# Performance work log

Measured on AMD Instinct MI355X. Metric: run time of the kernel, lower is better.

## Reference

```python
import jax, jax.numpy as jnp
import numpy as np

T = 2048           # tokens (single prefill sequence)
HIDDEN = 2048
H = 16             # num heads
D_NOPE = 128
D_ROPE = 64
D_V = 128
KV_LORA = 512
EPS = 1e-6
ROPE_THETA = 10000.0


def setup_inputs() -> dict:
    key = jax.random.key(0)
    ks = jax.random.split(key, 7)
    s = 0.02
    return {
        "positions": jnp.arange(T, dtype=jnp.int64) if jax.config.jax_enable_x64 else jnp.arange(T, dtype=jnp.int32),
        "hidden_states": jax.random.normal(ks[0], (T, HIDDEN), dtype=jnp.float32),
        "w_q": jax.random.normal(ks[1], (HIDDEN, H * (D_NOPE + D_ROPE)), dtype=jnp.float32) * s,
        "w_kv_a": jax.random.normal(ks[2], (HIDDEN, KV_LORA + D_ROPE), dtype=jnp.float32) * s,
        "kv_a_ln_w": jax.random.uniform(ks[3], (KV_LORA,), dtype=jnp.float32, minval=0.5, maxval=1.5),
        "w_kv_b": jax.random.normal(ks[4], (KV_LORA, H * (D_NOPE + D_V)), dtype=jnp.float32) * s,
        "w_o": jax.random.normal(ks[5], (H * D_V, HIDDEN), dtype=jnp.float32) * s,
    }


def _rms_norm(x, w):
    var = jnp.mean(jnp.square(x), axis=-1, keepdims=True)
    return x * jax.lax.rsqrt(var + EPS) * w


def _rope_nonneox(x, positions):
    # x: [..., D_ROPE], GPT-J (interleaved) style rotation
    inv_freq = 1.0 / (ROPE_THETA ** (jnp.arange(0, D_ROPE, 2, dtype=jnp.float32) / D_ROPE))
    freqs = positions.astype(jnp.float32)[:, None] * inv_freq  # [T, D_ROPE//2]
    cos, sin = jnp.cos(freqs), jnp.sin(freqs)
    # broadcast over head dim if present
    while cos.ndim < x.ndim:
        cos, sin = cos[:, None], sin[:, None]
    x1, x2 = x[..., 0::2], x[..., 1::2]
    o1 = x1 * cos - x2 * sin
    o2 = x2 * cos + x1 * sin
    return jnp.stack([o1, o2], axis=-1).reshape(x.shape)


def reference(positions, hidden_states, w_q, w_kv_a, kv_a_ln_w, w_kv_b, w_o):
    scaling = (D_NOPE + D_ROPE) ** -0.5
    # q projection (q_lora_rank is None branch)
    q = (hidden_states @ w_q).reshape(T, H, D_NOPE + D_ROPE)
    q_nope, q_pe = q[..., :D_NOPE], q[..., D_NOPE:]
    # compressed KV latent
    latent = hidden_states @ w_kv_a                 # [T, KV_LORA + D_ROPE]
    kv_a = _rms_norm(latent[:, :KV_LORA], kv_a_ln_w)
    k_pe = latent[:, KV_LORA:]                      # [T, D_ROPE], shared across heads
    # decompress to per-head k_nope and v (kv_b_proj)
    kv = (kv_a @ w_kv_b).reshape(T, H, D_NOPE + D_V)
    k_nope, v = kv[..., :D_NOPE], kv[..., D_NOPE:]
    # non-neox RoPE
    q_pe = _rope_nonneox(q_pe, positions)
    k_pe = _rope_nonneox(k_pe, positions)           # [T, D_ROPE]
    # concat rope parts (k_pe broadcast over heads)
    q_full = jnp.concatenate([q_nope, q_pe], axis=-1)                         # [T,H,192]
    k_full = jnp.concatenate([k_nope, jnp.broadcast_to(k_pe[:, None, :], (T, H, D_ROPE))], axis=-1)
    # causal MHA
    scores = jnp.einsum("qhd,khd->hqk", q_full, k_full) * scaling
    causal = positions[:, None] >= positions[None, :]
    scores = jnp.where(causal[None], scores, -jnp.inf)
    attn = jax.nn.softmax(scores, axis=-1)
    out = jnp.einsum("hqk,khd->qhd", attn, v).reshape(T, H * D_V)
    return out @ w_o
```

## Files before the change

### kernel.cpp

```cpp
#include <hip/hip_runtime.h>
#include <hip/hip_bf16.h>
#include <stdint.h>

#define T_SEQ   2048
#define NHEAD   16
#define NPAD1   3712

typedef short bf16x8  __attribute__((ext_vector_type(8)));
typedef float f32x4   __attribute__((ext_vector_type(4)));
typedef float f32x16  __attribute__((ext_vector_type(16)));

__device__ __forceinline__ unsigned short f2bf(float f) {
  union { float f; uint32_t u; } v; v.f = f;
  uint32_t u = v.u;
  uint32_t r = u + 0x7FFF + ((u >> 16) & 1);
  return (unsigned short)(r >> 16);
}

__device__ __forceinline__ void async16(const void* g, void* l) {
  __builtin_amdgcn_global_load_lds(
      (const __attribute__((address_space(1))) void*)g,
      (__attribute__((address_space(3))) void*)l, 16, 0, 0);
}

__device__ __forceinline__ void tr32(const float* __restrict__ in,
    unsigned short* __restrict__ out, int R, int C, int bx, int by,
    float (*tile)[33], int tid) {
  int r0 = bx * 32, c0 = by * 32;
  int tx = tid & 31, ty = tid >> 5;
  for (int i = 0; i < 4; i++)
    tile[ty + i * 8][tx] = in[(size_t)(r0 + ty + i * 8) * C + c0 + tx];
  __syncthreads();
  for (int i = 0; i < 4; i++) {
    int c = ty + i * 8;
    out[(size_t)(c0 + c) * R + r0 + tx] = f2bf(tile[tx][c]);
  }
}

__global__ __launch_bounds__(256) void prep_kernel(
    const float* __restrict__ hs, const float* __restrict__ w_q,
    const float* __restrict__ w_kv_a, const float* __restrict__ w_kv_b,
    const float* __restrict__ w_o, const int* __restrict__ positions,
    unsigned short* __restrict__ hs_bf, unsigned short* __restrict__ wcat_t,
    unsigned short* __restrict__ wkvb_t, unsigned short* __restrict__ wo_t,
    float* __restrict__ rope_tab) {
  __shared__ float tile[32][33];
  int bid = blockIdx.x, tid = threadIdx.x;
  if (bid < 4096) {
    int i = (bid * 256 + tid) * 4;
    float4 v = *(const float4*)(hs + i);
    ushort4 o; o.x = f2bf(v.x); o.y = f2bf(v.y); o.z = f2bf(v.z); o.w = f2bf(v.w);
    *(ushort4*)(hs_bf + i) = o;
  } else if (bid < 4096 + 6144) {
    int l = bid - 4096;
    tr32(w_q, wcat_t, 2048, 3072, l & 63, l >> 6, tile, tid);
  } else if (bid < 4096 + 6144 + 1152) {
    int l = bid - (4096 + 6144);
    tr32(w_kv_a, wcat_t + (size_t)3072 * 2048, 2048, 576, l & 63, l >> 6, tile, tid);
  } else if (bid < 4096 + 6144 + 1152 + 2048) {
    int l = bid - (4096 + 6144 + 1152);
    tr32(w_kv_b, wkvb_t, 512, 4096, l & 15, l >> 4, tile, tid);
  } else if (bid < 4096 + 6144 + 1152 + 2048 + 4096) {
    int l = bid - (4096 + 6144 + 1152 + 2048);
    tr32(w_o, wo_t, 2048, 2048, l & 63, l >> 6, tile, tid);
  } else if (bid < 17600) {
    int l = bid - (4096 + 6144 + 1152 + 2048 + 4096);
    uint4 z = (uint4){0, 0, 0, 0};
    *(uint4*)(wcat_t + (size_t)3648 * 2048 + (size_t)(l * 256 + tid) * 8) = z;
  } else {
    int l = bid - 17600;
    int t = l * 8 + (tid >> 5), p = tid & 31;
    float pos = (float)positions[t];
    float inv_freq = powf(10000.f, -(float)(2 * p) / 64.f);
    float c, s; sincosf(pos * inv_freq, &s, &c);
    rope_tab[(size_t)t * 64 + 2 * p]     = c;
    rope_tab[(size_t)t * 64 + 2 * p + 1] = s;
  }
}

template<int TM, int EPI>
__global__ __launch_bounds__(256) void gemm_bt_kernel(
    const unsigned short* __restrict__ A, const unsigned short* __restrict__ B,
    void* __restrict__ Cv, int M, int N, int K,
    unsigned short* __restrict__ q_full, const float* __restrict__ rope_tab) {
  constexpr int MT = TM / 32;
  __shared__ __align__(16) unsigned short Asm[2][TM * 64];
  __shared__ __align__(16) unsigned short Bsm[2][128 * 64];
  int tid = threadIdx.x, wid = tid >> 6, lane = tid & 63;
  int lrow = lane & 15, lquad = lane >> 4;
  int m0 = blockIdx.x * TM, n0 = blockIdx.y * 128;
  int wm = (wid & 1) * (TM / 2), wn = (wid >> 1) * 64;

  int row_s = tid >> 3;
  int cc_s = (tid & 7) ^ (row_s & 7);
  const unsigned short* Ag[MT];
  const unsigned short* Bg[4];
  #pragma unroll
  for (int p = 0; p < MT; p++) Ag[p] = A + (size_t)(m0 + row_s + p * 32) * K + cc_s * 8;
  #pragma unroll
  for (int p = 0; p < 4; p++)  Bg[p] = B + (size_t)(n0 + row_s + p * 32) * K + cc_s * 8;

  f32x4 acc[MT][4];
  #pragma unroll
  for (int i = 0; i < MT; i++)
    #pragma unroll
    for (int j = 0; j < 4; j++) acc[i][j] = (f32x4){0.f,0.f,0.f,0.f};

  #pragma unroll
  for (int p = 0; p < MT; p++) async16(Ag[p], &Asm[0][(tid + p * 256) * 8]);
  #pragma unroll
  for (int p = 0; p < 4; p++)  async16(Bg[p], &Bsm[0][(tid + p * 256) * 8]);

  int cur = 0;
  for (int k0 = 0; k0 < K; k0 += 64) {
    __syncthreads();
    if (k0 + 64 < K) {
      int nxt = cur ^ 1, kk = k0 + 64;
      #pragma unroll
      for (int p = 0; p < MT; p++) async16(Ag[p] + kk, &Asm[nxt][(tid + p * 256) * 8]);
      #pragma unroll
      for (int p = 0; p < 4; p++)  async16(Bg[p] + kk, &Bsm[nxt][(tid + p * 256) * 8]);
    }
    const unsigned short* As = Asm[cur];
    const unsigned short* Bs = Bsm[cur];
    int xr = (lrow & 7);
    #pragma unroll
    for (int kk = 0; kk < 2; kk++) {
      int cz = ((kk * 4 + lquad) ^ xr) * 8;
      bf16x8 af[MT], bfr[4];
      #pragma unroll
      for (int mt = 0; mt < MT; mt++)
        af[mt] = *(const bf16x8*)(As + (wm + mt * 16 + lrow) * 64 + cz);
      #pragma unroll
      for (int nt = 0; nt < 4; nt++)
        bfr[nt] = *(const bf16x8*)(Bs + (wn + nt * 16 + lrow) * 64 + cz);
      #pragma unroll
      for (int mt = 0; mt < MT; mt++)
        #pragma unroll
        for (int nt = 0; nt < 4; nt++)
          acc[mt][nt] = __builtin_amdgcn_mfma_f32_16x16x32_bf16(af[mt], bfr[nt], acc[mt][nt], 0, 0, 0);
    }
    cur ^= 1;
  }

  if constexpr (EPI == 2) {
    const float scaling = 0.07216878364870323f;
    float* qlat = (float*)Cv;
    #pragma unroll
    for (int nt = 0; nt < 4; nt++) {
      int colb = n0 + wn + nt * 16;
      if (colb >= 3072) {
        int col = colb - 3072 + lrow;
        #pragma unroll
        for (int mt = 0; mt < MT; mt++) {
          int row = m0 + wm + mt * 16 + lquad * 4;
          #pragma unroll
          for (int r = 0; r < 4; r++)
            qlat[(size_t)(row + r) * 640 + col] = acc[mt][nt][r];
        }
      } else {
        int h = colb / 192;
        int hm = colb - h * 192;
        unsigned short* qh = q_full + (size_t)h * T_SEQ * 192;
        if (hm < 128) {
          #pragma unroll
          for (int mt = 0; mt < MT; mt++) {
            int row = m0 + wm + mt * 16 + lquad * 4;
            #pragma unroll
            for (int r = 0; r < 4; r++)
              qh[(size_t)(row + r) * 192 + hm + lrow] = f2bf(acc[mt][nt][r] * scaling);
          }
        } else {
          int p2 = (hm - 128 + lrow) & ~1;
          int odd = lrow & 1;
          #pragma unroll
          for (int mt = 0; mt < MT; mt++) {
            int row = m0 + wm + mt * 16 + lquad * 4;
            #pragma unroll
            for (int r = 0; r < 4; r++) {
              int rg = row + r;
              float c = rope_tab[(size_t)rg * 64 + p2];
              float s = rope_tab[(size_t)rg * 64 + p2 + 1];
              float own = acc[mt][nt][r];
              float oth = __shfl_xor(own, 1, 64);
              float o = odd ? (own * c + oth * s)
                            : (own * c - oth * s);
              qh[(size_t)rg * 192 + hm + lrow] = f2bf(o * scaling);
            }
          }
        }
      }
    }
  } else {
    #pragma unroll
    for (int mt = 0; mt < MT; mt++)
      #pragma unroll
      for (int nt = 0; nt < 4; nt++) {
        int row = m0 + wm + mt * 16 + lquad * 4;
        int col = n0 + wn + nt * 16 + lrow;
        #pragma unroll
        for (int r = 0; r < 4; r++) {
          if (EPI == 1)
            ((unsigned short*)Cv)[(size_t)(row + r) * N + col] = f2bf(acc[mt][nt][r]);
          else
            ((float*)Cv)[(size_t)(row + r) * N + col] = acc[mt][nt][r];
        }
      }
  }
}

__global__ __launch_bounds__(256) void postproc1_kernel(
    const float* __restrict__ q_lat,
    const float* __restrict__ ln_w,
    const float* __restrict__ rope_tab,
    unsigned short* __restrict__ kv_a,
    unsigned short* __restrict__ k_pe)
{
  int t = blockIdx.x, tid = threadIdx.x;
  const float* row = q_lat + (size_t)t * 640;

  float v0 = row[tid], v1 = row[256 + tid];
  float ss = v0 * v0 + v1 * v1;
  for (int m = 1; m < 64; m <<= 1) ss += __shfl_xor(ss, m, 64);
  __shared__ float red[4];
  if ((tid & 63) == 0) red[tid >> 6] = ss;
  __shared__ float kro[64];
  if (tid < 32) {
    float c = rope_tab[(size_t)t * 64 + 2 * tid];
    float s = rope_tab[(size_t)t * 64 + 2 * tid + 1];
    float x1 = row[512 + 2 * tid], x2 = row[512 + 2 * tid + 1];
    kro[2 * tid]     = x1 * c - x2 * s;
    kro[2 * tid + 1] = x2 * c + x1 * s;
  }
  __syncthreads();
  float rstd = rsqrtf((red[0] + red[1] + red[2] + red[3]) * (1.f / 512.f) + 1e-6f);
  kv_a[(size_t)t * 512 + tid]       = f2bf(v0 * rstd * ln_w[tid]);
  kv_a[(size_t)t * 512 + 256 + tid] = f2bf(v1 * rstd * ln_w[256 + tid]);
  if (tid < 64) k_pe[(size_t)t * 64 + tid] = f2bf(kro[tid]);
}

__global__ __launch_bounds__(256) void kvpost_kernel(
    const unsigned short* __restrict__ kv_b,
    unsigned short* __restrict__ v_t) {
  __shared__ unsigned short tile[32][41];
  int l = blockIdx.x, tid = threadIdx.x;
  int h = l >> 8, t0 = (l & 63) * 32, d0 = ((l >> 6) & 3) * 32;
  int tx = tid & 31, ty = tid >> 5;
  for (int i = 0; i < 4; i++)
    tile[ty + i * 8][tx] = kv_b[(size_t)(t0 + ty + i * 8) * 4096 + h * 256 + 128 + d0 + tx];
  __syncthreads();
  for (int i = 0; i < 4; i++)
    v_t[((size_t)h * 128 + d0 + ty + i * 8) * T_SEQ + t0 + tx] = tile[tx][ty + i * 8];
}

#define PP 76
__global__ __launch_bounds__(256, 2) void flash_kernel(
    const unsigned short* __restrict__ q_full,
    const unsigned short* __restrict__ kv_b,
    const unsigned short* __restrict__ k_pe,
    const unsigned short* __restrict__ v_t,
    unsigned short* __restrict__ attn_out)
{
  __shared__ __align__(16) unsigned short Ksm[2][1536 * 8];
  __shared__ __align__(16) unsigned short Vsm[1024 * 8];
  __shared__ __align__(16) unsigned short Psm[64 * PP];
  __shared__ float Lred[2][64];
  int h = blockIdx.x;
  int y = blockIdx.y;
  int qb = (y < 16) ? (31 - y) : (y - 16);
  int tid = threadIdx.x, wid = tid >> 6, lane = tid & 63;
  int l31 = lane & 31, l5 = lane >> 5, x7 = l31 & 7;
  int rq = wid & 1, kq = wid >> 1;

  const unsigned short* vh = v_t + (size_t)h * 128 * T_SEQ;

  const unsigned short* pK[6]; int sK[6];
  #pragma unroll
  for (int j = 0; j < 6; j++) {
    int s = tid + j * 256, row = s / 24, cm = s - row * 24;
    int c = cm ^ (row & 7);
    if (c < 16) { pK[j] = kv_b + (size_t)row * 4096 + h * 256 + c * 8; sK[j] = 64 * 4096; }
    else        { pK[j] = k_pe + (size_t)row * 64 + (c - 16) * 8;      sK[j] = 64 * 64; }
  }
  int gV[4];
  #pragma unroll
  for (int j = 0; j < 4; j++) {
    int s = tid + j * 256, d = s >> 3;
    gV[j] = d * T_SEQ + ((s & 7) ^ (d & 7)) * 8;
  }
  int kxo[12];
  #pragma unroll
  for (int kc = 0; kc < 12; kc++)
    kxo[kc] = (kq * 32 + l31) * 192 + ((kc * 2 + l5) ^ x7) * 8;
  int vxb[2];
  #pragma unroll
  for (int ntv = 0; ntv < 2; ntv++) vxb[ntv] = (kq * 64 + ntv * 32 + l31) * 64;

  bf16x8 qf[12];
  {
    const unsigned short* qrow =
        q_full + ((size_t)h * T_SEQ + qb * 64 + rq * 32 + l31) * 192 + l5 * 8;
    #pragma unroll
    for (int kc = 0; kc < 12; kc++) qf[kc] = *(const bf16x8*)(qrow + kc * 16);
  }
  f32x16 oacc[2];
  for (int i = 0; i < 2; i++) oacc[i] = (f32x16)(0.f);
  float lsum[16];
  #pragma unroll
  for (int r = 0; r < 16; r++) lsum[r] = 0.f;
  int rl[16];
  #pragma unroll
  for (int r = 0; r < 16; r++) rl[r] = (r & 3) + 8 * (r >> 2) + 4 * l5;

  #pragma unroll
  for (int j = 0; j < 6; j++) async16(pK[j], &Ksm[0][(tid + j * 256) * 8]);

  int cur = 0;
  for (int kb = 0; kb <= qb; kb++) {
    __syncthreads();
    {
      const unsigned short* vb = vh + kb * 64;
      #pragma unroll
      for (int j = 0; j < 4; j++) async16(vb + gV[j], &Vsm[(tid + j * 256) * 8]);
    }
    const unsigned short* Ks = Ksm[cur];
    f32x16 sacc = (f32x16)(0.f);
    #pragma unroll
    for (int kc = 0; kc < 12; kc++) {
      bf16x8 kf = *(const bf16x8*)(Ks + kxo[kc]);
      sacc = __builtin_amdgcn_mfma_f32_32x32x16_bf16(qf[kc], kf, sacc, 0, 0, 0);
    }
    if (kb == qb) {
      int col_g = kb * 64 + kq * 32 + l31;
      int row_b = qb * 64 + rq * 32;
      #pragma unroll
      for (int r = 0; r < 16; r++)
        if (col_g > row_b + rl[r]) sacc[r] = -1e30f;
    }
    #pragma unroll
    for (int r = 0; r < 16; r++) {
      float p = __expf(sacc[r]);
      sacc[r] = p;
      lsum[r] += p;
    }
    #pragma unroll
    for (int r = 0; r < 16; r++)
      Psm[(rq * 32 + rl[r]) * PP + kq * 32 + l31] = f2bf(sacc[r]);
    __syncthreads();
    if (kb < qb) {
      #pragma unroll
      for (int j = 0; j < 6; j++)
        async16(pK[j] + (size_t)(kb + 1) * sK[j], &Ksm[cur ^ 1][(tid + j * 256) * 8]);
    }
    #pragma unroll
    for (int kc = 0; kc < 4; kc++) {
      bf16x8 pf = *(const bf16x8*)(Psm + (rq * 32 + l31) * PP + kc * 16 + l5 * 8);
      #pragma unroll
      for (int ntv = 0; ntv < 2; ntv++) {
        bf16x8 vf = *(const bf16x8*)(Vsm + vxb[ntv] + ((kc * 2 + l5) ^ x7) * 8);
        oacc[ntv] = __builtin_amdgcn_mfma_f32_32x32x16_bf16(pf, vf, oacc[ntv], 0, 0, 0);
      }
    }
    cur ^= 1;
  }

  #pragma unroll
  for (int r = 0; r < 16; r++) {
    float s = lsum[r];
    s += __shfl_xor(s, 1, 64);
    s += __shfl_xor(s, 2, 64);
    s += __shfl_xor(s, 4, 64);
    s += __shfl_xor(s, 8, 64);
    s += __shfl_xor(s, 16, 64);
    lsum[r] = s;
  }
  if (l31 == 0)
    #pragma unroll
    for (int r = 0; r < 16; r++) Lred[kq][rq * 32 + rl[r]] = lsum[r];
  __syncthreads();
  #pragma unroll
  for (int r = 0; r < 16; r++) {
    int row_l = rq * 32 + rl[r];
    float inv = 1.f / (Lred[0][row_l] + Lred[1][row_l]);
    int row_g = qb * 64 + row_l;
    #pragma unroll
    for (int ntv = 0; ntv < 2; ntv++)
      attn_out[(size_t)row_g * 2048 + h * 128 + kq * 64 + ntv * 32 + l31] =
          f2bf(oacc[ntv][r] * inv);
  }
}

extern "C" void kernel_launch(void* const* d_in, const int* in_sizes, int n_in,
                              void* d_out, int out_size, void* d_ws, size_t ws_size,
                              hipStream_t stream) {
  const int*   positions = (const int*)d_in[0];
  const float* hs     = (const float*)d_in[1];
  const float* w_q    = (const float*)d_in[2];
  const float* w_kv_a = (const float*)d_in[3];
  const float* ln_w   = (const float*)d_in[4];
  const float* w_kv_b = (const float*)d_in[5];
  const float* w_o    = (const float*)d_in[6];
  float* out = (float*)d_out;

  char* ws = (char*)d_ws;
  size_t off = 0;
  auto alloc = [&](size_t bytes) { void* p = ws + off; off += (bytes + 255) & ~(size_t)255; return p; };
  unsigned short* hs_bf   = (unsigned short*)alloc((size_t)2048 * 2048 * 2);
  unsigned short* wcat_t  = (unsigned short*)alloc((size_t)NPAD1 * 2048 * 2);
  float*          q_lat   = (float*)alloc((size_t)2048 * 640 * 4);
  unsigned short* kv_a_bf = (unsigned short*)alloc((size_t)2048 * 512 * 2);
  unsigned short* wkvb_t  = (unsigned short*)alloc((size_t)4096 * 512 * 2);
  unsigned short* kv_b    = (unsigned short*)alloc((size_t)2048 * 4096 * 2);
  unsigned short* q_full  = (unsigned short*)alloc((size_t)NHEAD * 2048 * 192 * 2);
  unsigned short* k_pe    = (unsigned short*)alloc((size_t)2048 * 64 * 2);
  unsigned short* v_t     = (unsigned short*)alloc((size_t)NHEAD * 128 * 2048 * 2);
  unsigned short* attn_o  = (unsigned short*)alloc((size_t)2048 * 2048 * 2);
  unsigned short* wo_t    = (unsigned short*)alloc((size_t)2048 * 2048 * 2);
  float*          rope_tab= (float*)alloc((size_t)2048 * 64 * 4);

  prep_kernel<<<17856, 256, 0, stream>>>(hs, w_q, w_kv_a, w_kv_b, w_o, positions,
                                         hs_bf, wcat_t, wkvb_t, wo_t, rope_tab);
  gemm_bt_kernel<128, 2><<<dim3(16, 29), 256, 0, stream>>>(
      hs_bf, wcat_t, q_lat, 2048, NPAD1, 2048, q_full, rope_tab);
  postproc1_kernel<<<2048, 256, 0, stream>>>(q_lat, ln_w, rope_tab, kv_a_bf, k_pe);
  gemm_bt_kernel<128, 1><<<dim3(16, 32), 256, 0, stream>>>(
      kv_a_bf, wkvb_t, kv_b, 2048, 4096, 512, nullptr, nullptr);
  kvpost_kernel<<<4096, 256, 0, stream>>>(kv_b, v_t);
  flash_kernel<<<dim3(16, 32), 256, 0, stream>>>(q_full, kv_b, k_pe, v_t, attn_o);
  gemm_bt_kernel<64, 0><<<dim3(32, 16), 256, 0, stream>>>(
      attn_o, wo_t, out, 2048, 2048, 2048, nullptr, nullptr);
}
```

Baseline: 252.7 us.

## Split long causal query blocks across two workgroups with partial-sum combine

```diff
diff --git a/kernel.cpp b/kernel.cpp
--- a/kernel.cpp
+++ b/kernel.cpp
@@ -254,20 +254,30 @@
 }
 
 #define PP 76
+#define PSTRIDE 8256
 __global__ __launch_bounds__(256, 2) void flash_kernel(
     const unsigned short* __restrict__ q_full,
     const unsigned short* __restrict__ kv_b,
     const unsigned short* __restrict__ k_pe,
     const unsigned short* __restrict__ v_t,
-    unsigned short* __restrict__ attn_out)
+    unsigned short* __restrict__ attn_out,
+    float* __restrict__ part)
 {
   __shared__ __align__(16) unsigned short Ksm[2][1536 * 8];
   __shared__ __align__(16) unsigned short Vsm[1024 * 8];
   __shared__ __align__(16) unsigned short Psm[64 * PP];
   __shared__ float Lred[2][64];
   int h = blockIdx.x;
-  int y = blockIdx.y;
-  int qb = (y < 16) ? (31 - y) : (y - 16);
+  int j = blockIdx.y;
+  int qb, k0t, k1t, pidx;
+  if (j < 32) {
+    qb = 16 + (j >> 1);
+    int mid = (qb + 1) >> 1;
+    if (j & 1) { k0t = mid; k1t = qb + 1; } else { k0t = 0; k1t = mid; }
+    pidx = (h * 16 + (qb - 16)) * 2 + (j & 1);
+  } else {
+    qb = 47 - j; k0t = 0; k1t = qb + 1; pidx = -1;
+  }
   int tid = threadIdx.x, wid = tid >> 6, lane = tid & 63;
   int l31 = lane & 31, l5 = lane >> 5, x7 = l31 & 7;
   int rq = wid & 1, kq = wid >> 1;
@@ -276,17 +286,17 @@
 
   const unsigned short* pK[6]; int sK[6];
   #pragma unroll
-  for (int j = 0; j < 6; j++) {
-    int s = tid + j * 256, row = s / 24, cm = s - row * 24;
+  for (int j2 = 0; j2 < 6; j2++) {
+    int s = tid + j2 * 256, row = s / 24, cm = s - row * 24;
     int c = cm ^ (row & 7);
-    if (c < 16) { pK[j] = kv_b + (size_t)row * 4096 + h * 256 + c * 8; sK[j] = 64 * 4096; }
-    else        { pK[j] = k_pe + (size_t)row * 64 + (c - 16) * 8;      sK[j] = 64 * 64; }
+    if (c < 16) { pK[j2] = kv_b + (size_t)row * 4096 + h * 256 + c * 8; sK[j2] = 64 * 4096; }
+    else        { pK[j2] = k_pe + (size_t)row * 64 + (c - 16) * 8;      sK[j2] = 64 * 64; }
   }
   int gV[4];
   #pragma unroll
-  for (int j = 0; j < 4; j++) {
-    int s = tid + j * 256, d = s >> 3;
-    gV[j] = d * T_SEQ + ((s & 7) ^ (d & 7)) * 8;
+  for (int j2 = 0; j2 < 4; j2++) {
+    int s = tid + j2 * 256, d = s >> 3;
+    gV[j2] = d * T_SEQ + ((s & 7) ^ (d & 7)) * 8;
   }
   int kxo[12];
   #pragma unroll
@@ -313,15 +323,16 @@
   for (int r = 0; r < 16; r++) rl[r] = (r & 3) + 8 * (r >> 2) + 4 * l5;
 
   #pragma unroll
-  for (int j = 0; j < 6; j++) async16(pK[j], &Ksm[0][(tid + j * 256) * 8]);
+  for (int j2 = 0; j2 < 6; j2++)
+    async16(pK[j2] + (size_t)k0t * sK[j2], &Ksm[0][(tid + j2 * 256) * 8]);
 
   int cur = 0;
-  for (int kb = 0; kb <= qb; kb++) {
+  for (int kb = k0t; kb < k1t; kb++) {
     __syncthreads();
     {
       const unsigned short* vb = vh + kb * 64;
       #pragma unroll
-      for (int j = 0; j < 4; j++) async16(vb + gV[j], &Vsm[(tid + j * 256) * 8]);
+      for (int j2 = 0; j2 < 4; j2++) async16(vb + gV[j2], &Vsm[(tid + j2 * 256) * 8]);
     }
     const unsigned short* Ks = Ksm[cur];
     f32x16 sacc = (f32x16)(0.f);
@@ -347,10 +358,10 @@
     for (int r = 0; r < 16; r++)
       Psm[(rq * 32 + rl[r]) * PP + kq * 32 + l31] = f2bf(sacc[r]);
     __syncthreads();
-    if (kb < qb) {
-      #pragma unroll
-      for (int j = 0; j < 6; j++)
-        async16(pK[j] + (size_t)(kb + 1) * sK[j], &Ksm[cur ^ 1][(tid + j * 256) * 8]);
+    if (kb + 1 < k1t) {
+      #pragma unroll
+      for (int j2 = 0; j2 < 6; j2++)
+        async16(pK[j2] + (size_t)(kb + 1) * sK[j2], &Ksm[cur ^ 1][(tid + j2 * 256) * 8]);
     }
     #pragma unroll
     for (int kc = 0; kc < 4; kc++) {
@@ -378,15 +389,49 @@
     #pragma unroll
     for (int r = 0; r < 16; r++) Lred[kq][rq * 32 + rl[r]] = lsum[r];
   __syncthreads();
-  #pragma unroll
-  for (int r = 0; r < 16; r++) {
-    int row_l = rq * 32 + rl[r];
-    float inv = 1.f / (Lred[0][row_l] + Lred[1][row_l]);
-    int row_g = qb * 64 + row_l;
-    #pragma unroll
-    for (int ntv = 0; ntv < 2; ntv++)
-      attn_out[(size_t)row_g * 2048 + h * 128 + kq * 64 + ntv * 32 + l31] =
-          f2bf(oacc[ntv][r] * inv);
+  if (pidx < 0) {
+    #pragma unroll
+    for (int r = 0; r < 16; r++) {
+      int row_l = rq * 32 + rl[r];
+      float inv = 1.f / (Lred[0][row_l] + Lred[1][row_l]);
+      int row_g = qb * 64 + row_l;
+      #pragma unroll
+      for (int ntv = 0; ntv < 2; ntv++)
+        attn_out[(size_t)row_g * 2048 + h * 128 + kq * 64 + ntv * 32 + l31] =
+            f2bf(oacc[ntv][r] * inv);
+    }
+  } else {
+    float* pb = part + (size_t)pidx * PSTRIDE;
+    #pragma unroll
+    for (int r = 0; r < 16; r++) {
+      int row_l = rq * 32 + rl[r];
+      #pragma unroll
+      for (int ntv = 0; ntv < 2; ntv++)
+        pb[row_l * 128 + kq * 64 + ntv * 32 + l31] = oacc[ntv][r];
+    }
+    if (tid < 64) pb[8192 + tid] = Lred[0][tid] + Lred[1][tid];
+  }
+}
+
+__global__ __launch_bounds__(256) void combine_kernel(
+    const float* __restrict__ part, unsigned short* __restrict__ attn_out) {
+  int bx = blockIdx.x;
+  int h = bx >> 4, q16 = bx & 15, qb = 16 + q16;
+  size_t b0 = (size_t)((h * 16 + q16) * 2) * PSTRIDE;
+  size_t b1 = b0 + PSTRIDE;
+  __shared__ float Ls[64];
+  int tid = threadIdx.x;
+  if (tid < 64) Ls[tid] = part[b0 + 8192 + tid] + part[b1 + 8192 + tid];
+  __syncthreads();
+  for (int i = tid; i < 2048; i += 256) {
+    float4 a = *(const float4*)(part + b0 + (size_t)i * 4);
+    float4 c = *(const float4*)(part + b1 + (size_t)i * 4);
+    int row = i >> 5;
+    float inv = 1.f / Ls[row];
+    ushort4 o;
+    o.x = f2bf((a.x + c.x) * inv); o.y = f2bf((a.y + c.y) * inv);
+    o.z = f2bf((a.z + c.z) * inv); o.w = f2bf((a.w + c.w) * inv);
+    *(ushort4*)(attn_out + (size_t)(qb * 64 + row) * 2048 + h * 128 + (i & 31) * 4) = o;
   }
 }
 
@@ -417,6 +462,7 @@
   unsigned short* attn_o  = (unsigned short*)alloc((size_t)2048 * 2048 * 2);
   unsigned short* wo_t    = (unsigned short*)alloc((size_t)2048 * 2048 * 2);
   float*          rope_tab= (float*)alloc((size_t)2048 * 64 * 4);
+  float*          part    = (float*)alloc((size_t)512 * PSTRIDE * 4);
 
   prep_kernel<<<17856, 256, 0, stream>>>(hs, w_q, w_kv_a, w_kv_b, w_o, positions,
                                          hs_bf, wcat_t, wkvb_t, wo_t, rope_tab);
@@ -426,7 +472,8 @@
   gemm_bt_kernel<128, 1><<<dim3(16, 32), 256, 0, stream>>>(
       kv_a_bf, wkvb_t, kv_b, 2048, 4096, 512, nullptr, nullptr);
   kvpost_kernel<<<4096, 256, 0, stream>>>(kv_b, v_t);
-  flash_kernel<<<dim3(16, 32), 256, 0, stream>>>(q_full, kv_b, k_pe, v_t, attn_o);
+  flash_kernel<<<dim3(16, 48), 256, 0, stream>>>(q_full, kv_b, k_pe, v_t, attn_o, part);
+  combine_kernel<<<256, 256, 0, stream>>>(part, attn_o);
   gemm_bt_kernel<64, 0><<<dim3(32, 16), 256, 0, stream>>>(
       attn_o, wo_t, out, 2048, 2048, 2048, nullptr, nullptr);
 }
```

Result: slower. 262.5 us (+3.9%).
